# Kernel tuning notes

Hardware: AMD Instinct MI355X
Metric: run time of the kernel (lower is better)

Reference implementation:

```python
import jax, jax.numpy as jnp
import numpy as np

DIM, HEADS = 512, 8
HD = DIM // HEADS
B, T = 1, 512


def _rope_tables(T, hd):
    inv_freq = 1.0 / (10000.0 ** (jnp.arange(0, hd, 2, dtype=jnp.float32) / hd))
    freqs = jnp.arange(T, dtype=jnp.float32)[:, None] * inv_freq[None, :]
    emb = jnp.concatenate([freqs, freqs], axis=-1)  # [T, hd]
    return jnp.cos(emb), jnp.sin(emb)


def _rotate_half_heads(x):
    # Faithful to source: torch chunk(2, dim=1) on [B,H,hd,1,T] splits the HEADS axis.
    x1, x2 = jnp.split(x, 2, axis=1)
    return jnp.concatenate([-x2, x1], axis=1)


def setup_inputs():
    key = jax.random.key(0)
    ks = jax.random.split(key, 5)
    s = 1.0 / np.sqrt(DIM)
    return {
        "x": jax.random.normal(ks[0], (B, T, DIM), dtype=jnp.float32),
        "Wq": jax.random.normal(ks[1], (DIM, DIM), dtype=jnp.float32) * s,
        "Wk": jax.random.normal(ks[2], (DIM, DIM), dtype=jnp.float32) * s,
        "Wv": jax.random.normal(ks[3], (DIM, DIM), dtype=jnp.float32) * s,
        "Wo": jax.random.normal(ks[4], (DIM, DIM), dtype=jnp.float32) * s,
    }


def reference(x, Wq, Wk, Wv, Wo):
    b, t, d = x.shape
    h, hd = HEADS, d // HEADS
    scale = 1.0 / np.sqrt(hd)

    def proj(W):
        # 1x1 Conv2d == per-position linear; channel o = head*hd + c  -> [B,H,hd,T]
        return jnp.einsum('btd,od->bot', x, W).reshape(b, h, hd, t)

    q, k, v = proj(Wq), proj(Wk), proj(Wv)

    cos, sin = _rope_tables(t, hd)
    cosT = cos.T[None, None]  # [1,1,hd,T]
    sinT = sin.T[None, None]
    q = q * cosT + _rotate_half_heads(q) * sinT
    k = k * cosT + _rotate_half_heads(k) * sinT

    # Per-channel outer-product scores (inner dim of the matmul is the singleton axis)
    att = jnp.einsum('bhci,bhcj->bhcij', q, k) * scale  # [B,H,hd,T,T]
    causal_mask = jnp.triu(jnp.ones((t, t), dtype=bool), k=1)
    att = jnp.where(causal_mask, -jnp.inf, att)
    att = jax.nn.softmax(att, axis=-1)

    out = jnp.einsum('bhcij,bhcj->bhci', att, v).reshape(b, d, t)
    return jnp.einsum('od,bdt->bto', Wo, out)  # [B,T,D]
```

## Files before the change

### kernel.cpp

```cpp
#include <hip/hip_runtime.h>
#include <math.h>

typedef __attribute__((ext_vector_type(8))) short short8;
typedef __attribute__((ext_vector_type(4))) float floatx4;

__device__ __forceinline__ unsigned short f2bf(float f) {
    unsigned int u = __builtin_bit_cast(unsigned int, f);
    u += 0x7FFFu + ((u >> 16) & 1u);
    return (unsigned short)(u >> 16);
}


__global__ __launch_bounds__(256) void cvt_bf16(
    const float* __restrict__ x,  const float* __restrict__ Wq,
    const float* __restrict__ Wk, const float* __restrict__ Wv,
    const float* __restrict__ Wo, unsigned short* __restrict__ Wallb,
    unsigned short* __restrict__ xb, unsigned short* __restrict__ Wob)
{
    const float* src; unsigned short* dst;
    switch (blockIdx.y) {
        case 0: src = Wq; dst = Wallb;          break;
        case 1: src = Wk; dst = Wallb + 262144; break;
        case 2: src = Wv; dst = Wallb + 524288; break;
        case 3: src = x;  dst = xb;             break;
        default: src = Wo; dst = Wob;           break;
    }
    const int i4 = (blockIdx.x * 256 + threadIdx.x) * 4;
    const float4 v = *(const float4*)(src + i4);
    ushort4 o;
    o.x = f2bf(v.x); o.y = f2bf(v.y); o.z = f2bf(v.z); o.w = f2bf(v.w);
    *(ushort4*)(dst + i4) = o;
}

__global__ __launch_bounds__(64) void gemm_wave(
    const unsigned short* __restrict__ A, const unsigned short* __restrict__ B,
    float* __restrict__ C)
{
    const int lane = threadIdx.x;
    const int quad = lane >> 4, l15 = lane & 15;
    const int m0 = (blockIdx.x >> 4) * 32;
    const int n0 = (blockIdx.x & 15) * 32;

    const unsigned short* a0 = A + (m0 + l15) * 512 + quad * 8;
    const unsigned short* a1 = a0 + 16 * 512;
    const unsigned short* b0 = B + (n0 + l15) * 512 + quad * 8;
    const unsigned short* b1 = b0 + 16 * 512;

    floatx4 acc[2][2] = {{{0.f,0.f,0.f,0.f},{0.f,0.f,0.f,0.f}},
                         {{0.f,0.f,0.f,0.f},{0.f,0.f,0.f,0.f}}};

    short8 a0c = *(const short8*)(a0);      short8 a1c = *(const short8*)(a1);
    short8 b0c = *(const short8*)(b0);      short8 b1c = *(const short8*)(b1);
    short8 a0n = *(const short8*)(a0 + 32); short8 a1n = *(const short8*)(a1 + 32);
    short8 b0n = *(const short8*)(b0 + 32); short8 b1n = *(const short8*)(b1 + 32);

    #pragma unroll
    for (int kc = 0; kc < 512; kc += 32) {
        short8 a0f, a1f, b0f, b1f;
        if (kc + 64 < 512) {
            a0f = *(const short8*)(a0 + kc + 64); a1f = *(const short8*)(a1 + kc + 64);
            b0f = *(const short8*)(b0 + kc + 64); b1f = *(const short8*)(b1 + kc + 64);
        }
        acc[0][0] = __builtin_amdgcn_mfma_f32_16x16x32_bf16(a0c, b0c, acc[0][0], 0, 0, 0);
        acc[0][1] = __builtin_amdgcn_mfma_f32_16x16x32_bf16(a0c, b1c, acc[0][1], 0, 0, 0);
        acc[1][0] = __builtin_amdgcn_mfma_f32_16x16x32_bf16(a1c, b0c, acc[1][0], 0, 0, 0);
        acc[1][1] = __builtin_amdgcn_mfma_f32_16x16x32_bf16(a1c, b1c, acc[1][1], 0, 0, 0);
        a0c = a0n; a1c = a1n; b0c = b0n; b1c = b1n;
        a0n = a0f; a1n = a1f; b0n = b0f; b1n = b1f;
    }

    #pragma unroll
    for (int mt = 0; mt < 2; ++mt)
        #pragma unroll
        for (int nt = 0; nt < 2; ++nt) {
            const int grow = m0 + mt * 16 + quad * 4;
            const int gcol = n0 + nt * 16 + l15;
            #pragma unroll
            for (int r = 0; r < 4; ++r)
                C[(grow + r) * 512 + gcol] = acc[mt][nt][r];
        }
}

__global__ __launch_bounds__(256) void attn_rope2(
    const float* __restrict__ qkv, unsigned short* __restrict__ attTb)
{
    const int ch   = blockIdx.x;
    const int tid  = threadIdx.x;
    const int w    = tid >> 6;
    const int lane = tid & 63;
    const int p    = ch ^ 256;
    const float sgn = (ch < 256) ? -1.f : 1.f;

    __shared__ float ks_[512];
    __shared__ float vs_[512];
    __shared__ float cs_[512];
    __shared__ float sn_[512];

    const float* __restrict__ qg = qkv;
    const float* __restrict__ kg = qkv + 262144;
    const float* __restrict__ vg = qkv + 524288;

    const float inv_freq = powf(10000.f, -(float)(ch & 31) * (1.f / 32.f));

    #pragma unroll
    for (int h = 0; h < 2; ++h) {
        const int t = tid + h * 256;
        float sn, cs;
        sincosf((float)t * inv_freq, &sn, &cs);
        ks_[t] = (kg[ch * 512 + t] * cs + sgn * kg[p * 512 + t] * sn) * 0.125f;
        vs_[t] = vg[ch * 512 + t];
        cs_[t] = cs;
        sn_[t] = sn;
    }
    __syncthreads();

    const int i0 = tid, i1 = tid + 256;
    const float q0 = qg[ch * 512 + i0] * cs_[i0] + sgn * qg[p * 512 + i0] * sn_[i0];
    const float q1 = qg[ch * 512 + i1] * cs_[i1] + sgn * qg[p * 512 + i1] * sn_[i1];

    float l0 = 0.f, a0 = 0.f, l1 = 0.f, a1 = 0.f;
    const int jw = w * 64;

    for (int j = 0; j < jw; j += 4) {
        const float4 k4 = *(const float4*)&ks_[j];
        const float4 v4 = *(const float4*)&vs_[j];
        float e;
        e = __expf(q0 * k4.x); l0 += e; a0 = fmaf(e, v4.x, a0);
        e = __expf(q1 * k4.x); l1 += e; a1 = fmaf(e, v4.x, a1);
        e = __expf(q0 * k4.y); l0 += e; a0 = fmaf(e, v4.y, a0);
        e = __expf(q1 * k4.y); l1 += e; a1 = fmaf(e, v4.y, a1);
        e = __expf(q0 * k4.z); l0 += e; a0 = fmaf(e, v4.z, a0);
        e = __expf(q1 * k4.z); l1 += e; a1 = fmaf(e, v4.z, a1);
        e = __expf(q0 * k4.w); l0 += e; a0 = fmaf(e, v4.w, a0);
        e = __expf(q1 * k4.w); l1 += e; a1 = fmaf(e, v4.w, a1);
    }
    #pragma unroll
    for (int jj = 0; jj < 64; jj += 4) {
        const float4 k4 = *(const float4*)&ks_[jw + jj];
        const float4 v4 = *(const float4*)&vs_[jw + jj];
        float e;
        e = (jj + 0 <= lane) ? __expf(q0 * k4.x) : 0.f; l0 += e; a0 = fmaf(e, v4.x, a0);
        e = (jj + 1 <= lane) ? __expf(q0 * k4.y) : 0.f; l0 += e; a0 = fmaf(e, v4.y, a0);
        e = (jj + 2 <= lane) ? __expf(q0 * k4.z) : 0.f; l0 += e; a0 = fmaf(e, v4.z, a0);
        e = (jj + 3 <= lane) ? __expf(q0 * k4.w) : 0.f; l0 += e; a0 = fmaf(e, v4.w, a0);
        e = __expf(q1 * k4.x); l1 += e; a1 = fmaf(e, v4.x, a1);
        e = __expf(q1 * k4.y); l1 += e; a1 = fmaf(e, v4.y, a1);
        e = __expf(q1 * k4.z); l1 += e; a1 = fmaf(e, v4.z, a1);
        e = __expf(q1 * k4.w); l1 += e; a1 = fmaf(e, v4.w, a1);
    }
    for (int j = jw + 64; j < 256 + jw; j += 4) {
        const float4 k4 = *(const float4*)&ks_[j];
        const float4 v4 = *(const float4*)&vs_[j];
        float e;
        e = __expf(q1 * k4.x); l1 += e; a1 = fmaf(e, v4.x, a1);
        e = __expf(q1 * k4.y); l1 += e; a1 = fmaf(e, v4.y, a1);
        e = __expf(q1 * k4.z); l1 += e; a1 = fmaf(e, v4.z, a1);
        e = __expf(q1 * k4.w); l1 += e; a1 = fmaf(e, v4.w, a1);
    }
    #pragma unroll
    for (int jj = 0; jj < 64; jj += 4) {
        const float4 k4 = *(const float4*)&ks_[256 + jw + jj];
        const float4 v4 = *(const float4*)&vs_[256 + jw + jj];
        float e;
        e = (jj + 0 <= lane) ? __expf(q1 * k4.x) : 0.f; l1 += e; a1 = fmaf(e, v4.x, a1);
        e = (jj + 1 <= lane) ? __expf(q1 * k4.y) : 0.f; l1 += e; a1 = fmaf(e, v4.y, a1);
        e = (jj + 2 <= lane) ? __expf(q1 * k4.z) : 0.f; l1 += e; a1 = fmaf(e, v4.z, a1);
        e = (jj + 3 <= lane) ? __expf(q1 * k4.w) : 0.f; l1 += e; a1 = fmaf(e, v4.w, a1);
    }

    attTb[i0 * 512 + ch] = f2bf(a0 / l0);
    attTb[i1 * 512 + ch] = f2bf(a1 / l1);
}

extern "C" void kernel_launch(void* const* d_in, const int* in_sizes, int n_in,
                              void* d_out, int out_size, void* d_ws, size_t ws_size,
                              hipStream_t stream)
{
    const float* x  = (const float*)d_in[0];
    const float* Wq = (const float*)d_in[1];
    const float* Wk = (const float*)d_in[2];
    const float* Wv = (const float*)d_in[3];
    const float* Wo = (const float*)d_in[4];
    float* out = (float*)d_out;

    unsigned short* Wallb = (unsigned short*)d_ws;
    unsigned short* xb    = Wallb + 786432;
    unsigned short* Wob   = xb + 262144;
    unsigned short* attTb = Wob + 262144;
    float* qkvf = (float*)(attTb + 262144);

    cvt_bf16<<<dim3(256, 5), 256, 0, stream>>>(x, Wq, Wk, Wv, Wo, Wallb, xb, Wob);
    gemm_wave<<<768, 64, 0, stream>>>(Wallb, xb, qkvf);
    attn_rope2<<<512, 256, 0, stream>>>(qkvf, attTb);
    gemm_wave<<<256, 64, 0, stream>>>(attTb, Wob, out);
}
```

Baseline: 106.4 us.

## Replace single-wave GEMM with LDS-tiled 64x64 block GEMM using direct-to-LDS loads

The one-wave-per-32x32-tile GEMM, which read bf16 operands straight from global memory into registers, is replaced by a 256-thread block that computes a 64x64 tile. Each 64-wide K slice of A and B is staged into shared memory with global_load_lds, using an XOR swizzle on 16-byte chunks to avoid bank conflicts. The four waves then share these tiles for their MFMA work. This cuts redundant global operand traffic, but it launches far fewer blocks (192 and 64) and adds two barriers per K step with no double buffering.

```diff
diff --git a/kernel.cpp b/kernel.cpp
--- a/kernel.cpp
+++ b/kernel.cpp
@@ -32,49 +32,79 @@
     *(ushort4*)(dst + i4) = o;
 }
 
-__global__ __launch_bounds__(64) void gemm_wave(
-    const unsigned short* __restrict__ A, const unsigned short* __restrict__ B,
+__global__ __launch_bounds__(256) void gemm_bt(
+    const unsigned short* __restrict__ A,
+    const unsigned short* __restrict__ B,
     float* __restrict__ C)
 {
-    const int lane = threadIdx.x;
-    const int quad = lane >> 4, l15 = lane & 15;
-    const int m0 = (blockIdx.x >> 4) * 32;
-    const int n0 = (blockIdx.x & 15) * 32;
-
-    const unsigned short* a0 = A + (m0 + l15) * 512 + quad * 8;
-    const unsigned short* a1 = a0 + 16 * 512;
-    const unsigned short* b0 = B + (n0 + l15) * 512 + quad * 8;
-    const unsigned short* b1 = b0 + 16 * 512;
+    __shared__ unsigned short As[64 * 64];
+    __shared__ unsigned short Bs[64 * 64];
+
+    const int tid  = threadIdx.x;
+    const int lane = tid & 63;
+    const int w    = tid >> 6;
+    const int m0   = blockIdx.y * 64;
+    const int n0   = blockIdx.x * 64;
+    const int wm   = (w >> 1) * 32;
+    const int wn   = (w & 1) * 32;
+
+    const int srow8 = w * 8 + (lane >> 3);
+    const int c8    = lane & 7;
 
     floatx4 acc[2][2] = {{{0.f,0.f,0.f,0.f},{0.f,0.f,0.f,0.f}},
                          {{0.f,0.f,0.f,0.f},{0.f,0.f,0.f,0.f}}};
 
-    short8 a0c = *(const short8*)(a0);      short8 a1c = *(const short8*)(a1);
-    short8 b0c = *(const short8*)(b0);      short8 b1c = *(const short8*)(b1);
-    short8 a0n = *(const short8*)(a0 + 32); short8 a1n = *(const short8*)(a1 + 32);
-    short8 b0n = *(const short8*)(b0 + 32); short8 b1n = *(const short8*)(b1 + 32);
-
-    #pragma unroll
-    for (int kc = 0; kc < 512; kc += 32) {
-        short8 a0f, a1f, b0f, b1f;
-        if (kc + 64 < 512) {
-            a0f = *(const short8*)(a0 + kc + 64); a1f = *(const short8*)(a1 + kc + 64);
-            b0f = *(const short8*)(b0 + kc + 64); b1f = *(const short8*)(b1 + kc + 64);
+    const int quad = lane >> 4;
+    const int l15  = lane & 15;
+
+    for (int kc = 0; kc < 512; kc += 64) {
+        #pragma unroll
+        for (int rr = 0; rr < 2; ++rr) {
+            const int row  = rr * 32 + srow8;
+            const int gcol = kc + ((c8 ^ (row & 7)) * 8);
+            const unsigned short* ga = A + (m0 + row) * 512 + gcol;
+            const unsigned short* gb = B + (n0 + row) * 512 + gcol;
+            __builtin_amdgcn_global_load_lds(
+                (const __attribute__((address_space(1))) void*)ga,
+                (__attribute__((address_space(3))) void*)&As[(rr * 32 + w * 8) * 64],
+                16, 0, 0);
+            __builtin_amdgcn_global_load_lds(
+                (const __attribute__((address_space(1))) void*)gb,
+                (__attribute__((address_space(3))) void*)&Bs[(rr * 32 + w * 8) * 64],
+                16, 0, 0);
         }
-        acc[0][0] = __builtin_amdgcn_mfma_f32_16x16x32_bf16(a0c, b0c, acc[0][0], 0, 0, 0);
-        acc[0][1] = __builtin_amdgcn_mfma_f32_16x16x32_bf16(a0c, b1c, acc[0][1], 0, 0, 0);
-        acc[1][0] = __builtin_amdgcn_mfma_f32_16x16x32_bf16(a1c, b0c, acc[1][0], 0, 0, 0);
-        acc[1][1] = __builtin_amdgcn_mfma_f32_16x16x32_bf16(a1c, b1c, acc[1][1], 0, 0, 0);
-        a0c = a0n; a1c = a1n; b0c = b0n; b1c = b1n;
-        a0n = a0f; a1n = a1f; b0n = b0f; b1n = b1f;
+        __syncthreads();
+
+        #pragma unroll
+        for (int ks = 0; ks < 2; ++ks) {
+            const int cIdx = ks * 4 + quad;
+            short8 a[2], b[2];
+            #pragma unroll
+            for (int mt = 0; mt < 2; ++mt) {
+                const int row = wm + mt * 16 + l15;
+                a[mt] = *(const short8*)&As[row * 64 + ((cIdx ^ (row & 7)) * 8)];
+            }
+            #pragma unroll
+            for (int nt = 0; nt < 2; ++nt) {
+                const int row = wn + nt * 16 + l15;
+                b[nt] = *(const short8*)&Bs[row * 64 + ((cIdx ^ (row & 7)) * 8)];
+            }
+            #pragma unroll
+            for (int mt = 0; mt < 2; ++mt)
+                #pragma unroll
+                for (int nt = 0; nt < 2; ++nt)
+                    acc[mt][nt] = __builtin_amdgcn_mfma_f32_16x16x32_bf16(
+                        a[mt], b[nt], acc[mt][nt], 0, 0, 0);
+        }
+        __syncthreads();
     }
 
     #pragma unroll
     for (int mt = 0; mt < 2; ++mt)
         #pragma unroll
         for (int nt = 0; nt < 2; ++nt) {
-            const int grow = m0 + mt * 16 + quad * 4;
-            const int gcol = n0 + nt * 16 + l15;
+            const int grow = m0 + wm + mt * 16 + quad * 4;
+            const int gcol = n0 + wn + nt * 16 + l15;
             #pragma unroll
             for (int r = 0; r < 4; ++r)
                 C[(grow + r) * 512 + gcol] = acc[mt][nt][r];
@@ -82,7 +112,7 @@
 }
 
 __global__ __launch_bounds__(256) void attn_rope2(
-    const float* __restrict__ qkv, unsigned short* __restrict__ attTb)
+    const float* __restrict__ qkv, unsigned short* __restrict__ attb)
 {
     const int ch   = blockIdx.x;
     const int tid  = threadIdx.x;
@@ -168,8 +198,8 @@
         e = (jj + 3 <= lane) ? __expf(q1 * k4.w) : 0.f; l1 += e; a1 = fmaf(e, v4.w, a1);
     }
 
-    attTb[i0 * 512 + ch] = f2bf(a0 / l0);
-    attTb[i1 * 512 + ch] = f2bf(a1 / l1);
+    attb[i0 * 512 + ch] = f2bf(a0 / l0);
+    attb[i1 * 512 + ch] = f2bf(a1 / l1);
 }
 
 extern "C" void kernel_launch(void* const* d_in, const int* in_sizes, int n_in,
@@ -186,11 +216,11 @@
     unsigned short* Wallb = (unsigned short*)d_ws;
     unsigned short* xb    = Wallb + 786432;
     unsigned short* Wob   = xb + 262144;
-    unsigned short* attTb = Wob + 262144;
-    float* qkvf = (float*)(attTb + 262144);
+    unsigned short* attb  = Wob + 262144;
+    float* qkvf = (float*)(attb + 262144);
 
     cvt_bf16<<<dim3(256, 5), 256, 0, stream>>>(x, Wq, Wk, Wv, Wo, Wallb, xb, Wob);
-    gemm_wave<<<768, 64, 0, stream>>>(Wallb, xb, qkvf);
-    attn_rope2<<<512, 256, 0, stream>>>(qkvf, attTb);
-    gemm_wave<<<256, 64, 0, stream>>>(attTb, Wob, out);
-}
+    gemm_bt<<<dim3(8, 24), 256, 0, stream>>>(Wallb, xb, qkvf);
+    attn_rope2<<<512, 256, 0, stream>>>(qkvf, attb);
+    gemm_bt<<<dim3(8, 8), 256, 0, stream>>>(attb, Wob, out);
+}
```

After: 106.7 us. About the same (+0.3%).
